# Kernel tuning notes

Hardware: AMD Instinct MI355X
Metric: run time of the kernel (lower is better)

## Reference

```python
import jax, jax.numpy as jnp
import numpy as np

IMG = 64
STEPS = 10
UNITS = 256
PATCH_DIM = (IMG // 2) * (IMG // 2) * 9  # 3x3 patches, stride 2, SAME
ENC_IN = PATCH_DIM + 2 * UNITS  # read_window (patch+h_dec) concat h_dec again


def lstm_cell(x, h, c, kernel, rec, bias):
    # Keras LSTMCell gate order: i, f, g(candidate), o
    z = x @ kernel + h @ rec + bias
    i, f, g, o = jnp.split(z, 4, axis=-1)
    c_new = jax.nn.sigmoid(f) * c + jax.nn.sigmoid(i) * jnp.tanh(g)
    h_new = jax.nn.sigmoid(o) * jnp.tanh(c_new)
    return h_new, c_new


def extract_patches(img):
    # img: [B, H, W] -> 3x3 patches, stride 2, SAME -> [B, (H/2)*(W/2)*9]
    p = jax.lax.conv_general_dilated_patches(
        img[:, None, :, :], (3, 3), (2, 2), 'SAME')  # [B, 9, H/2, W/2]
    p = jnp.transpose(p, (0, 2, 3, 1))  # TF extract_patches layout [B,H',W',9]
    return p.reshape(img.shape[0], -1)


def setup_inputs() -> dict:
    key = jax.random.key(0)
    ks = jax.random.split(key, 8)
    B = 512
    s = 0.05  # small init scale to avoid gate saturation
    return {
        'x': jax.random.uniform(ks[0], (B, IMG, IMG), dtype=jnp.float32),
        'enc_kernel': jax.random.normal(ks[1], (ENC_IN, 4 * UNITS), dtype=jnp.float32) * s,
        'enc_rec': jax.random.normal(ks[2], (UNITS, 4 * UNITS), dtype=jnp.float32) * s,
        'enc_bias': jnp.zeros((4 * UNITS,), jnp.float32),
        'dec_kernel': jax.random.normal(ks[3], (UNITS, 4 * UNITS), dtype=jnp.float32) * s,
        'dec_rec': jax.random.normal(ks[4], (UNITS, 4 * UNITS), dtype=jnp.float32) * s,
        'dec_bias': jnp.zeros((4 * UNITS,), jnp.float32),
        'W_enc': jax.random.normal(ks[5], (UNITS, 10), dtype=jnp.float32) * s,
        'b_enc': jnp.zeros((10,), jnp.float32),
        'W_dec': jax.random.normal(ks[6], (UNITS, IMG * IMG), dtype=jnp.float32) * s,
        'b_dec': jnp.zeros((IMG * IMG,), jnp.float32),
    }


def reference(x, enc_kernel, enc_rec, enc_bias, dec_kernel, dec_rec, dec_bias,
              W_enc, b_enc, W_dec, b_dec):
    B = x.shape[0]
    canvas0 = jnp.zeros((B, IMG, IMG), x.dtype)
    h_enc0 = c_enc0 = h_dec0 = c_dec0 = jnp.zeros((B, UNITS), x.dtype)

    def step(carry, _):
        canvas, h_enc, c_enc, h_dec, c_dec = carry
        x_hat = x - jax.nn.sigmoid(canvas)                      # error image
        patches = extract_patches(x_hat)                        # [B, PATCH_DIM]
        read_window = jnp.concatenate([patches, h_dec], axis=1)
        enc_in = jnp.concatenate([read_window, h_dec], axis=1)  # [B, ENC_IN]
        h_enc, c_enc = lstm_cell(enc_in, h_enc, c_enc, enc_kernel, enc_rec, enc_bias)
        # attention over 10 slots; glimpse vector as attn-weighted slot embeddings
        attn = jax.nn.softmax(h_enc @ W_enc + b_enc, axis=1)    # [B, 10]
        z = attn @ W_enc.T                                      # [B, UNITS]
        h_dec, c_dec = lstm_cell(z, h_dec, c_dec, dec_kernel, dec_rec, dec_bias)
        canvas = canvas + (h_dec @ W_dec + b_dec).reshape(B, IMG, IMG)
        return (canvas, h_enc, c_enc, h_dec, c_dec), None

    (canvas, _, _, _, _), _ = jax.lax.scan(
        step, (canvas0, h_enc0, c_enc0, h_dec0, c_dec0), None, length=STEPS)
    return canvas
```

## Files before the change

### kernel.cpp

```cpp
#include <hip/hip_runtime.h>

typedef unsigned short ushort_t;
typedef __attribute__((ext_vector_type(8))) short short8;
typedef __attribute__((ext_vector_type(4))) float floatx4;
typedef __attribute__((ext_vector_type(4))) unsigned int uintx4;

#define BSZ   512
#define UNITS 256
#define IMG   64
#define STEPS 10
#define GATES 1024
#define KENC  4608
#define NBLK  256
#define BK 32
#define FLAG_STRIDE 32

__device__ inline float b2f(ushort_t u) {
  union { float f; unsigned int i; } v; v.i = ((unsigned int)u) << 16; return v.f;
}
__device__ inline ushort_t f2b(float f) {
  unsigned int u = __float_as_uint(f);
  u += 0x7fffu + ((u >> 16) & 1u);
  return (ushort_t)(u >> 16);
}
__device__ inline float sigm(float x) { return 1.f / (1.f + __expf(-x)); }

#define GLL(g, l) __builtin_amdgcn_global_load_lds(                      \
    (const __attribute__((address_space(1))) void*)(g),                  \
    (__attribute__((address_space(3))) void*)(l), 16, 0, 0)

#define CLOADF(p)    __hip_atomic_load((p), __ATOMIC_RELAXED, __HIP_MEMORY_SCOPE_AGENT)
#define CSTOREF(p,v) __hip_atomic_store((p), (v), __ATOMIC_RELAXED, __HIP_MEMORY_SCOPE_AGENT)
#define CSTOREU(p,v) __hip_atomic_store((p), (ushort_t)(v), __ATOMIC_RELAXED, __HIP_MEMORY_SCOPE_AGENT)

__device__ inline uintx4 cload16(const ushort_t* p) {
  uintx4 r;
  asm volatile("global_load_dwordx4 %0, %1, off sc0 sc1" : "=v"(r) : "v"(p));
  return r;
}
__device__ inline void waitvm0() {
  asm volatile("s_waitcnt vmcnt(0)" ::: "memory");
}
__device__ inline unsigned ldsaddr(const ushort_t* p) {
  return (unsigned)(unsigned long long)(const __attribute__((address_space(3))) void*)p;
}
__device__ inline void dsw16(unsigned off, uintx4 v) {
  asm volatile("ds_write_b128 %0, %1" :: "v"(off), "v"(v));
}

__device__ inline void gridbar(unsigned* bar, unsigned id) {
  __syncthreads();
  const int b = blockIdx.x, t = threadIdx.x;
  unsigned* gen = bar + NBLK * FLAG_STRIDE;
  if (b == 0) {
    if (t > 0 && t < NBLK) {
      while (__hip_atomic_load(bar + t * FLAG_STRIDE, __ATOMIC_RELAXED,
                               __HIP_MEMORY_SCOPE_AGENT) < id)
        __builtin_amdgcn_s_sleep(1);
    }
    __syncthreads();
    if (t == 0)
      __hip_atomic_store(gen, id, __ATOMIC_RELAXED, __HIP_MEMORY_SCOPE_AGENT);
  } else if (t == 0) {
    __hip_atomic_store(bar + b * FLAG_STRIDE, id, __ATOMIC_RELAXED,
                       __HIP_MEMORY_SCOPE_AGENT);
    while (__hip_atomic_load(gen, __ATOMIC_RELAXED,
                             __HIP_MEMORY_SCOPE_AGENT) < id)
      __builtin_amdgcn_s_sleep(1);
  }
  __syncthreads();
}

__global__ __launch_bounds__(256) void k_prep_pix(const float* __restrict__ ek,
                                                  ushort_t* __restrict__ ohi) {
  __shared__ float T[64][68];
  int t = threadIdx.x;
  int pix0 = blockIdx.x * 64, n0 = blockIdx.y * 64;
  int r = t >> 2, seg = t & 3;
  int pix = pix0 + r;
  int ri = pix >> 6, ci = pix & 63;
  float4 acc4[4];
#pragma unroll
  for (int j = 0; j < 4; ++j) acc4[j] = float4{0.f, 0.f, 0.f, 0.f};
#pragma unroll
  for (int di = 0; di < 3; ++di) {
    int ii = ri - di;
    if (ii < 0 || (ii & 1)) continue;
    int oi = ii >> 1;  if (oi >= 32) continue;
#pragma unroll
    for (int dj = 0; dj < 3; ++dj) {
      int jj = ci - dj;
      if (jj < 0 || (jj & 1)) continue;
      int oj = jj >> 1;  if (oj >= 32) continue;
      const float* row = ek + (size_t)((oi * 32 + oj) * 9 + di * 3 + dj) * GATES
                         + n0 + seg * 16;
#pragma unroll
      for (int j = 0; j < 4; ++j) {
        float4 v = *(const float4*)(row + j * 4);
        acc4[j].x += v.x; acc4[j].y += v.y; acc4[j].z += v.z; acc4[j].w += v.w;
      }
    }
  }
#pragma unroll
  for (int j = 0; j < 4; ++j) *(float4*)&T[r][seg * 16 + j * 4] = acc4[j];
  __syncthreads();
  ushort_t thi[16];
#pragma unroll
  for (int j = 0; j < 16; ++j) thi[j] = f2b(T[seg * 16 + j][r]);
  size_t off = (size_t)(n0 + r) * KENC + pix0 + seg * 16;
  *(uint4*)(ohi + off)     = *(const uint4*)&thi[0];
  *(uint4*)(ohi + off + 8) = *(const uint4*)&thi[8];
}

__global__ __launch_bounds__(256) void k_prep_multi(
    const float* __restrict__ ek, const float* __restrict__ er,
    const float* __restrict__ dk, const float* __restrict__ dr,
    const float* __restrict__ Wdec,
    ushort_t* __restrict__ Wet_hi,
    ushort_t* __restrict__ Wdt_hi, ushort_t* __restrict__ Wdt_lo,
    ushort_t* __restrict__ Wct_hi, ushort_t* __restrict__ Wct_lo,
    unsigned* __restrict__ bar) {
  __shared__ float T[64][68];
  int t = threadIdx.x;
  int z = blockIdx.z;
  int k0 = blockIdx.x * 64, n0 = blockIdx.y * 64;
  int r = t >> 2, seg = t & 3;
  if (z == 0) {
    int fid = (blockIdx.y * 4 + blockIdx.x) * 256 + t;
    if (fid <= NBLK * FLAG_STRIDE) bar[fid] = 0u;
  }

  const float *s0, *s1 = nullptr;
  ushort_t *ohi, *olo = nullptr;
  int src_ld, out_ld, koff;
  if (z == 0) { s0 = ek + (size_t)9216 * GATES; s1 = ek + (size_t)9472 * GATES;
                src_ld = GATES; ohi = Wet_hi; out_ld = KENC; koff = 4096; }
  else if (z == 1) { s0 = er; src_ld = GATES; ohi = Wet_hi; out_ld = KENC; koff = 4352; }
  else if (z == 2) { s0 = dk; src_ld = GATES; ohi = Wdt_hi; olo = Wdt_lo; out_ld = 512; koff = 0; }
  else if (z == 3) { s0 = dr; src_ld = GATES; ohi = Wdt_hi; olo = Wdt_lo; out_ld = 512; koff = 256; }
  else { s0 = Wdec; src_ld = 4096; ohi = Wct_hi; olo = Wct_lo; out_ld = 256; koff = 0;
         n0 += (z - 4) * 1024; }

  const float* src = s0 + (size_t)(k0 + r) * src_ld + n0 + seg * 16;
  const float* src2 = s1 ? (s1 + (size_t)(k0 + r) * src_ld + n0 + seg * 16) : nullptr;
#pragma unroll
  for (int j = 0; j < 4; ++j) {
    float4 v = *(const float4*)(src + j * 4);
    if (src2) {
      float4 w = *(const float4*)(src2 + j * 4);
      v.x += w.x; v.y += w.y; v.z += w.z; v.w += w.w;
    }
    *(float4*)&T[r][seg * 16 + j * 4] = v;
  }
  __syncthreads();
  ushort_t thi[16], tlo[16];
#pragma unroll
  for (int j = 0; j < 16; ++j) {
    float v = T[seg * 16 + j][r];
    ushort_t h = f2b(v);
    thi[j] = h;
    tlo[j] = f2b(v - b2f(h));
  }
  size_t off = (size_t)(n0 + r) * out_ld + koff + k0 + seg * 16;
  *(uint4*)(ohi + off)     = *(const uint4*)&thi[0];
  *(uint4*)(ohi + off + 8) = *(const uint4*)&thi[8];
  if (olo) {
    *(uint4*)(olo + off)     = *(const uint4*)&tlo[0];
    *(uint4*)(olo + off + 8) = *(const uint4*)&tlo[8];
  }
}

__global__ __launch_bounds__(512, 2) void k_persist(
    const float* __restrict__ x,
    const float* __restrict__ ebias, const float* __restrict__ dbias,
    const float* __restrict__ Wenc, const float* __restrict__ benc,
    const float* __restrict__ bdec,
    float* __restrict__ canvas, float* __restrict__ c_enc, float* __restrict__ c_dec,
    float* __restrict__ zep,
    ushort_t* __restrict__ ehi, ushort_t* __restrict__ dhi, ushort_t* __restrict__ dlo,
    const ushort_t* __restrict__ Wet_hi,
    const ushort_t* __restrict__ Wdt_hi, const ushort_t* __restrict__ Wdt_lo,
    const ushort_t* __restrict__ Wct_hi, const ushort_t* __restrict__ Wct_lo,
    unsigned* bar) {
  __shared__ __align__(16) ushort_t smem[24576];
  const int b = blockIdx.x, t = threadIdx.x;
  const int lane = t & 63, w = t >> 6;
  const int q = lane >> 4, c16 = lane & 15;
  const int qs = (q ^ ((c16 >> 1) & 3)) * 8;
  const int half = t >> 8, u8 = t & 255;
  const int rrow = b * 2 + half;
  unsigned barid = 0;

  {
    const int cby = b >> 5, cbx = b & 31;
    float4* cv4 = (float4*)canvas;
    const float4 z4 = float4{0.f, 0.f, 0.f, 0.f};
#pragma unroll
    for (int j = 0; j < 4; ++j) {
      int idx = j * 512 + t;
      cv4[(size_t)(cby * 64 + (idx >> 5)) * 1024 + cbx * 32 + (idx & 31)] = z4;
    }
    c_enc[rrow * UNITS + u8] = 0.f;
    if (b < 128) {
      const int m0 = (b >> 3) * 32, u0 = (b & 7) * 32;
#pragma unroll
      for (int j = 0; j < 2; ++j) {
        int idx = j * 512 + t;
        c_dec[(m0 + (idx >> 5)) * UNITS + u0 + (idx & 31)] = 0.f;
      }
    }
    CSTOREU(ehi + (size_t)rrow * KENC + 4096 + u8, 0);
    CSTOREU(ehi + (size_t)rrow * KENC + 4352 + u8, 0);
    CSTOREU(dhi + (size_t)rrow * 512 + u8, 0);
    CSTOREU(dhi + (size_t)rrow * 512 + 256 + u8, 0);
    CSTOREU(dlo + (size_t)rrow * 512 + u8, 0);
    CSTOREU(dlo + (size_t)rrow * 512 + 256 + u8, 0);
    for (int pix = u8; pix < 4096; pix += 256)
      CSTOREU(ehi + (size_t)rrow * KENC + pix,
              f2b(x[(size_t)rrow * 4096 + pix] - 0.5f));
  }
  gridbar(bar, ++barid);

  for (int s = 0; s < STEPS; ++s) {
    {
      const int bm = b & 15, bu = (b >> 4) & 3, bz = b >> 6;
      const int m0 = bm * 32, u0 = bu * 64, kstart = bz * 1152;
      const int sseg = (t & 3) ^ ((t >> 3) & 3);
      const ushort_t* pA = ehi + (size_t)(m0 + ((t >> 2) & 31)) * KENC
                           + kstart + sseg * 8;
      const int br0 = t >> 2, br1 = 128 + (t >> 2);
      const int g0 = (br0 >> 6) * 256 + u0 + (br0 & 63);
      const int g1 = (br1 >> 6) * 256 + u0 + (br1 & 63);
      const ushort_t* pB0 = Wet_hi + (size_t)g0 * KENC + kstart + sseg * 8;
      const ushort_t* pB1 = Wet_hi + (size_t)g1 * KENC + kstart + sseg * 8;

      floatx4 acc[2][2];
#pragma unroll
      for (int i = 0; i < 2; ++i)
#pragma unroll
        for (int j = 0; j < 2; ++j) acc[i][j] = floatx4{0.f, 0.f, 0.f, 0.f};

      uintx4 va;
      if (t < 128) va = cload16(pA);
      GLL(pB0, &smem[1024 + t * 8]);
      GLL(pB1, &smem[5120 + t * 8]);
      pA += BK; pB0 += BK; pB1 += BK;
      waitvm0();
      if (t < 128) dsw16(ldsaddr(&smem[t * 8]), va);
      __syncthreads();
      for (int kt = 0; kt < 36; ++kt) {
        const int cur = (kt & 1) * 9216, nxt = 9216 - cur;
        if (kt + 1 < 36) {
          if (t < 128) va = cload16(pA);
          GLL(pB0, &smem[nxt + 1024 + t * 8]);
          GLL(pB1, &smem[nxt + 5120 + t * 8]);
          pA += BK; pB0 += BK; pB1 += BK;
        }
        short8 af[2], bf[2];
#pragma unroll
        for (int i = 0; i < 2; ++i)
          af[i] = *(const short8*)&smem[cur + (i * 16 + c16) * BK + qs];
#pragma unroll
        for (int j = 0; j < 2; ++j)
          bf[j] = *(const short8*)&smem[cur + 1024 + (w * 32 + j * 16 + c16) * BK + qs];
#pragma unroll
        for (int mi = 0; mi < 2; ++mi)
#pragma unroll
          for (int ni = 0; ni < 2; ++ni)
            acc[mi][ni] = __builtin_amdgcn_mfma_f32_16x16x32_bf16(af[mi], bf[ni], acc[mi][ni], 0, 0, 0);
        if (kt + 1 < 36) {
          waitvm0();
          if (t < 128) dsw16(ldsaddr(&smem[nxt + t * 8]), va);
        }
        __syncthreads();
      }
#pragma unroll
      for (int mi = 0; mi < 2; ++mi)
#pragma unroll
        for (int ni = 0; ni < 2; ++ni) {
          const int col = w * 32 + ni * 16 + c16;
          const int gcol = (col >> 6) * 256 + u0 + (col & 63);
          const int rowb = m0 + mi * 16 + q * 4;
#pragma unroll
          for (int r = 0; r < 4; ++r)
            CSTOREF(zep + ((size_t)(rowb + r) * 4 + bz) * 1024 + gcol, acc[mi][ni][r]);
        }
    }
    gridbar(bar, ++barid);

    {
      float* shf = (float*)smem;
      const float* rb = zep + (size_t)rrow * 4096 + u8;
      float v[16];
#pragma unroll
      for (int z = 0; z < 4; ++z)
#pragma unroll
        for (int g = 0; g < 4; ++g)
          v[z * 4 + g] = CLOADF(rb + z * 1024 + g * 256);
      float zi = ebias[u8], zf = ebias[u8 + 256];
      float zg = ebias[u8 + 512], zo = ebias[u8 + 768];
#pragma unroll
      for (int z = 0; z < 4; ++z) {
        zi += v[z * 4]; zf += v[z * 4 + 1]; zg += v[z * 4 + 2]; zo += v[z * 4 + 3];
      }
      float c = c_enc[rrow * UNITS + u8];
      float cn = sigm(zf) * c + sigm(zi) * tanhf(zg);
      float h = sigm(zo) * tanhf(cn);
      c_enc[rrow * UNITS + u8] = cn;
      CSTOREU(ehi + (size_t)rrow * KENC + 4352 + u8, f2b(h));
      shf[half * 256 + u8] = h;
      __syncthreads();
      if (u8 < 64) {
        float acc[10];
#pragma unroll
        for (int j = 0; j < 10; ++j) acc[j] = 0.f;
        for (int qq = 0; qq < 4; ++qq) {
          float hv = shf[half * 256 + u8 + qq * 64];
          const float* wr = Wenc + (u8 + qq * 64) * 10;
#pragma unroll
          for (int j = 0; j < 10; ++j) acc[j] += hv * wr[j];
        }
        for (int off = 32; off > 0; off >>= 1)
#pragma unroll
          for (int j = 0; j < 10; ++j) acc[j] += __shfl_down(acc[j], off);
        if (u8 == 0)
          for (int j = 0; j < 10; ++j) shf[512 + half * 10 + j] = acc[j] + benc[j];
      }
      __syncthreads();
      float mx = shf[512 + half * 10];
      for (int j = 1; j < 10; ++j) mx = fmaxf(mx, shf[512 + half * 10 + j]);
      float e[10], se = 0.f;
      for (int j = 0; j < 10; ++j) { e[j] = __expf(shf[512 + half * 10 + j] - mx); se += e[j]; }
      float inv = 1.f / se;
      const float* wr = Wenc + u8 * 10;
      float zzv = 0.f;
      for (int j = 0; j < 10; ++j) zzv += e[j] * inv * wr[j];
      ushort_t zh = f2b(zzv);
      CSTOREU(dhi + (size_t)rrow * 512 + u8, zh);
      CSTOREU(dlo + (size_t)rrow * 512 + u8, f2b(zzv - b2f(zh)));
    }
    gridbar(bar, ++barid);

    if (b < 128) {
      const int m0 = (b >> 3) * 32, u0 = (b & 7) * 32;
      const int wm = w >> 2, wn = w & 3;
      const int ta2 = t & 127;
      const int sseg = (ta2 & 3) ^ ((ta2 >> 3) & 3);
      const ushort_t* pA = ((t < 128) ? dhi : dlo)
                           + (size_t)(m0 + (ta2 >> 2)) * 512 + sseg * 8;
      const int brow = t >> 2;
      const int gD = (brow >> 5) * 256 + u0 + (brow & 31);
      const int bsegD = (t & 3) ^ ((t >> 3) & 3);
      const ushort_t* pBh = Wdt_hi + (size_t)gD * 512 + bsegD * 8;
      const ushort_t* pBl = Wdt_lo + (size_t)gD * 512 + bsegD * 8;
      const int dA = ((t < 128) ? 0 : 1024) + ta2 * 8;

      floatx4 acc[2];
      acc[0] = floatx4{0.f, 0.f, 0.f, 0.f};
      acc[1] = floatx4{0.f, 0.f, 0.f, 0.f};

      uintx4 va;
      if (t < 256) va = cload16(pA);
      GLL(pBh, &smem[2048 + t * 8]);
      GLL(pBl, &smem[6144 + t * 8]);
      pA += BK; pBh += BK; pBl += BK;
      waitvm0();
      if (t < 256) dsw16(ldsaddr(&smem[dA]), va);
      __syncthreads();
      for (int kt = 0; kt < 16; ++kt) {
        const int cur = (kt & 1) * 10240, nxt = 10240 - cur;
        if (kt + 1 < 16) {
          if (t < 256) va = cload16(pA);
          GLL(pBh, &smem[nxt + 2048 + t * 8]);
          GLL(pBl, &smem[nxt + 6144 + t * 8]);
          pA += BK; pBh += BK; pBl += BK;
        }
        short8 ah, al, bh[2], bl[2];
        {
          const int ra = (wm * 16 + c16) * BK + qs;
          ah = *(const short8*)&smem[cur + ra];
          al = *(const short8*)&smem[cur + 1024 + ra];
        }
#pragma unroll
        for (int i = 0; i < 2; ++i) {
          const int rb2 = (wn * 32 + i * 16 + c16) * BK + qs;
          bh[i] = *(const short8*)&smem[cur + 2048 + rb2];
          bl[i] = *(const short8*)&smem[cur + 6144 + rb2];
        }
#pragma unroll
        for (int ni = 0; ni < 2; ++ni) {
          acc[ni] = __builtin_amdgcn_mfma_f32_16x16x32_bf16(ah, bh[ni], acc[ni], 0, 0, 0);
          acc[ni] = __builtin_amdgcn_mfma_f32_16x16x32_bf16(ah, bl[ni], acc[ni], 0, 0, 0);
          acc[ni] = __builtin_amdgcn_mfma_f32_16x16x32_bf16(al, bh[ni], acc[ni], 0, 0, 0);
        }
        if (kt + 1 < 16) {
          waitvm0();
          if (t < 256) dsw16(ldsaddr(&smem[nxt + dA]), va);
        }
        __syncthreads();
      }
      float* zacc = (float*)smem;
#pragma unroll
      for (int ni = 0; ni < 2; ++ni) {
        const int col = wn * 32 + ni * 16 + c16;
        const int rowb = wm * 16 + q * 4;
#pragma unroll
        for (int r = 0; r < 4; ++r) zacc[(rowb + r) * 128 + col] = acc[ni][r];
      }
      __syncthreads();
#pragma unroll
      for (int j = 0; j < 2; ++j) {
        const int idx = j * 512 + t;
        const int row = idx >> 5, uu = idx & 31;
        const int un = u0 + uu, rg = m0 + row;
        float zi = zacc[row * 128 + uu]      + dbias[un];
        float zf = zacc[row * 128 + 32 + uu] + dbias[256 + un];
        float zg = zacc[row * 128 + 64 + uu] + dbias[512 + un];
        float zo = zacc[row * 128 + 96 + uu] + dbias[768 + un];
        float c = c_dec[rg * UNITS + un];
        float cn = sigm(zf) * c + sigm(zi) * tanhf(zg);
        float h = sigm(zo) * tanhf(cn);
        c_dec[rg * UNITS + un] = cn;
        ushort_t hh = f2b(h);
        CSTOREU(dhi + (size_t)rg * 512 + 256 + un, hh);
        CSTOREU(dlo + (size_t)rg * 512 + 256 + un, f2b(h - b2f(hh)));
        CSTOREU(ehi + (size_t)rg * KENC + 4096 + un, hh);
      }
    }
    gridbar(bar, ++barid);

    {
      const int by = b >> 5, bx = b & 31;
      const int m0 = by * 64, n0 = bx * 128;
      const int wm = w >> 2, wn = w & 3;
      const int ia = t & 255;
      const int aseg = ((ia & 3) ^ ((ia >> 3) & 3));
      const int bseg = ((t & 3) ^ ((t >> 3) & 3));
      const ushort_t* pA = ((t < 256) ? (dhi + 256) : (dlo + 256))
                           + (size_t)(m0 + (ia >> 2)) * 512 + aseg * 8;
      const ushort_t* pBh = Wct_hi + (size_t)(n0 + (t >> 2)) * 256 + bseg * 8;
      const ushort_t* pBl = Wct_lo + (size_t)(n0 + (t >> 2)) * 256 + bseg * 8;
      const int dA = ((t < 256) ? 0 : 2048) + ia * 8;

      floatx4 acc[2][2];
#pragma unroll
      for (int i = 0; i < 2; ++i)
#pragma unroll
        for (int j = 0; j < 2; ++j) acc[i][j] = floatx4{0.f, 0.f, 0.f, 0.f};

      uintx4 va = cload16(pA);
      GLL(pBh, &smem[4096 + t * 8]);
      GLL(pBl, &smem[8192 + t * 8]);
      pA += BK; pBh += BK; pBl += BK;
      waitvm0();
      dsw16(ldsaddr(&smem[dA]), va);
      __syncthreads();
      for (int kt = 0; kt < 8; ++kt) {
        const int cur = (kt & 1) * 12288, nxt = 12288 - cur;
        if (kt + 1 < 8) {
          va = cload16(pA);
          GLL(pBh, &smem[nxt + 4096 + t * 8]);
          GLL(pBl, &smem[nxt + 8192 + t * 8]);
          pA += BK; pBh += BK; pBl += BK;
        }
        short8 ah[2], al[2], bh[2], bl[2];
#pragma unroll
        for (int i = 0; i < 2; ++i) {
          const int ra = (wm * 32 + i * 16 + c16) * BK + qs;
          ah[i] = *(const short8*)&smem[cur + ra];
          al[i] = *(const short8*)&smem[cur + 2048 + ra];
          const int rb2 = (wn * 32 + i * 16 + c16) * BK + qs;
          bh[i] = *(const short8*)&smem[cur + 4096 + rb2];
          bl[i] = *(const short8*)&smem[cur + 8192 + rb2];
        }
#pragma unroll
        for (int mi = 0; mi < 2; ++mi)
#pragma unroll
          for (int ni = 0; ni < 2; ++ni) {
            acc[mi][ni] = __builtin_amdgcn_mfma_f32_16x16x32_bf16(ah[mi], bh[ni], acc[mi][ni], 0, 0, 0);
            acc[mi][ni] = __builtin_amdgcn_mfma_f32_16x16x32_bf16(ah[mi], bl[ni], acc[mi][ni], 0, 0, 0);
            acc[mi][ni] = __builtin_amdgcn_mfma_f32_16x16x32_bf16(al[mi], bh[ni], acc[mi][ni], 0, 0, 0);
          }
        if (kt + 1 < 8) {
          waitvm0();
          dsw16(ldsaddr(&smem[nxt + dA]), va);
        }
        __syncthreads();
      }
#pragma unroll
      for (int mi = 0; mi < 2; ++mi)
#pragma unroll
        for (int ni = 0; ni < 2; ++ni) {
          const int n = n0 + wn * 32 + ni * 16 + c16;
          const int mb = m0 + wm * 32 + mi * 16 + q * 4;
          const float bv = bdec[n];
#pragma unroll
          for (int r = 0; r < 4; ++r) {
            const int m = mb + r;
            const size_t idx = (size_t)m * 4096 + n;
            const float cv = canvas[idx] + acc[mi][ni][r] + bv;
            canvas[idx] = cv;
            CSTOREU(ehi + (size_t)m * KENC + n, f2b(x[idx] - sigm(cv)));
          }
        }
    }
    if (s + 1 < STEPS) gridbar(bar, ++barid);
  }
}

extern "C" void kernel_launch(void* const* d_in, const int* in_sizes, int n_in,
                              void* d_out, int out_size, void* d_ws, size_t ws_size,
                              hipStream_t stream) {
  const float* x     = (const float*)d_in[0];
  const float* ek    = (const float*)d_in[1];
  const float* er    = (const float*)d_in[2];
  const float* ebias = (const float*)d_in[3];
  const float* dk    = (const float*)d_in[4];
  const float* dr    = (const float*)d_in[5];
  const float* dbias = (const float*)d_in[6];
  const float* Wenc  = (const float*)d_in[7];
  const float* benc  = (const float*)d_in[8];
  const float* Wdec  = (const float*)d_in[9];
  const float* bdec  = (const float*)d_in[10];

  float* canvas = (float*)d_out;

  char* p = (char*)d_ws;
  float* c_enc  = (float*)p;        p += (size_t)BSZ * UNITS * 4;
  float* c_dec  = (float*)p;        p += (size_t)BSZ * UNITS * 4;
  float* zep    = (float*)p;        p += (size_t)4 * BSZ * GATES * 4;
  ushort_t* ehi = (ushort_t*)p;     p += (size_t)BSZ * KENC * 2;
  ushort_t* dhi = (ushort_t*)p;     p += (size_t)BSZ * 512 * 2;
  ushort_t* dlo = (ushort_t*)p;     p += (size_t)BSZ * 512 * 2;
  ushort_t* Wet_hi = (ushort_t*)p;  p += (size_t)GATES * KENC * 2;
  ushort_t* Wdt_hi = (ushort_t*)p;  p += (size_t)GATES * 512 * 2;
  ushort_t* Wdt_lo = (ushort_t*)p;  p += (size_t)GATES * 512 * 2;
  ushort_t* Wct_hi = (ushort_t*)p;  p += (size_t)4096 * UNITS * 2;
  ushort_t* Wct_lo = (ushort_t*)p;  p += (size_t)4096 * UNITS * 2;
  unsigned* bar = (unsigned*)p;     p += (size_t)(NBLK * FLAG_STRIDE + 16) * 4;

  k_prep_pix<<<dim3(64, 16), 256, 0, stream>>>(ek, Wet_hi);
  k_prep_multi<<<dim3(4, 16, 8), 256, 0, stream>>>(ek, er, dk, dr, Wdec,
                                                   Wet_hi, Wdt_hi, Wdt_lo,
                                                   Wct_hi, Wct_lo, bar);

  void* args[] = {(void*)&x, (void*)&ebias, (void*)&dbias, (void*)&Wenc,
                  (void*)&benc, (void*)&bdec, (void*)&canvas, (void*)&c_enc,
                  (void*)&c_dec, (void*)&zep, (void*)&ehi,
                  (void*)&dhi, (void*)&dlo, (void*)&Wet_hi, (void*)&Wdt_hi,
                  (void*)&Wdt_lo, (void*)&Wct_hi, (void*)&Wct_lo, (void*)&bar};
  if (hipLaunchCooperativeKernel((void*)k_persist, dim3(NBLK), dim3(512),
                                 args, 0, stream) != hipSuccess) {
    k_persist<<<dim3(NBLK), dim3(512), 0, stream>>>(
        x, ebias, dbias, Wenc, benc, bdec, canvas, c_enc, c_dec, zep,
        ehi, dhi, dlo, Wet_hi, Wdt_hi, Wdt_lo, Wct_hi, Wct_lo, bar);
  }
}
```

Baseline: 838.6 us.

## Retile persistent kernel GEMM phases for all blocks and vectorized gate reads

```diff
diff --git a/kernel.cpp b/kernel.cpp
--- a/kernel.cpp
+++ b/kernel.cpp
@@ -182,7 +182,7 @@
     const ushort_t* __restrict__ Wdt_hi, const ushort_t* __restrict__ Wdt_lo,
     const ushort_t* __restrict__ Wct_hi, const ushort_t* __restrict__ Wct_lo,
     unsigned* bar) {
-  __shared__ __align__(16) ushort_t smem[24576];
+  __shared__ __align__(16) ushort_t smem[36864];
   const int b = blockIdx.x, t = threadIdx.x;
   const int lane = t & 63, w = t >> 6;
   const int q = lane >> 4, c16 = lane & 15;
@@ -192,23 +192,16 @@
   unsigned barid = 0;
 
   {
-    const int cby = b >> 5, cbx = b & 31;
+    const int cm0 = (b >> 4) * 32, cn0 = (b & 15) * 64;
     float4* cv4 = (float4*)canvas;
     const float4 z4 = float4{0.f, 0.f, 0.f, 0.f};
 #pragma unroll
     for (int j = 0; j < 4; ++j) {
       int idx = j * 512 + t;
-      cv4[(size_t)(cby * 64 + (idx >> 5)) * 1024 + cbx * 32 + (idx & 31)] = z4;
+      cv4[(size_t)(cm0 + (idx >> 6)) * 1024 + cn0 + (idx & 63)] = z4;
     }
     c_enc[rrow * UNITS + u8] = 0.f;
-    if (b < 128) {
-      const int m0 = (b >> 3) * 32, u0 = (b & 7) * 32;
-#pragma unroll
-      for (int j = 0; j < 2; ++j) {
-        int idx = j * 512 + t;
-        c_dec[(m0 + (idx >> 5)) * UNITS + u0 + (idx & 31)] = 0.f;
-      }
-    }
+    c_dec[((b & 31) * 16 + (t >> 5)) * UNITS + (b >> 5) * 32 + (t & 31)] = 0.f;
     CSTOREU(ehi + (size_t)rrow * KENC + 4096 + u8, 0);
     CSTOREU(ehi + (size_t)rrow * KENC + 4352 + u8, 0);
     CSTOREU(dhi + (size_t)rrow * 512 + u8, 0);
@@ -223,86 +216,86 @@
 
   for (int s = 0; s < STEPS; ++s) {
     {
-      const int bm = b & 15, bu = (b >> 4) & 3, bz = b >> 6;
-      const int m0 = bm * 32, u0 = bu * 64, kstart = bz * 1152;
+      const int bm = b & 31, bu = (b >> 5) & 1, bz = b >> 6;
+      const int m0 = bm * 16, kstart = bz * 1152;
       const int sseg = (t & 3) ^ ((t >> 3) & 3);
-      const ushort_t* pA = ehi + (size_t)(m0 + ((t >> 2) & 31)) * KENC
-                           + kstart + sseg * 8;
-      const int br0 = t >> 2, br1 = 128 + (t >> 2);
-      const int g0 = (br0 >> 6) * 256 + u0 + (br0 & 63);
-      const int g1 = (br1 >> 6) * 256 + u0 + (br1 & 63);
-      const ushort_t* pB0 = Wet_hi + (size_t)g0 * KENC + kstart + sseg * 8;
-      const ushort_t* pB1 = Wet_hi + (size_t)g1 * KENC + kstart + sseg * 8;
-
-      floatx4 acc[2][2];
-#pragma unroll
-      for (int i = 0; i < 2; ++i)
-#pragma unroll
-        for (int j = 0; j < 2; ++j) acc[i][j] = floatx4{0.f, 0.f, 0.f, 0.f};
+      const ushort_t* pA = ehi + (size_t)(m0 + (t >> 2)) * KENC + kstart + sseg * 8;
+      const int br = t >> 2;
+      const ushort_t* pB[4];
+#pragma unroll
+      for (int c = 0; c < 4; ++c) {
+        const int r0 = c * 128 + br;
+        const int srow = (r0 >> 7) * 256 + bu * 128 + (r0 & 127);
+        pB[c] = Wet_hi + (size_t)srow * KENC + kstart + sseg * 8;
+      }
+
+      floatx4 acc[4];
+#pragma unroll
+      for (int j = 0; j < 4; ++j) acc[j] = floatx4{0.f, 0.f, 0.f, 0.f};
 
       uintx4 va;
-      if (t < 128) va = cload16(pA);
-      GLL(pB0, &smem[1024 + t * 8]);
-      GLL(pB1, &smem[5120 + t * 8]);
-      pA += BK; pB0 += BK; pB1 += BK;
+      if (t < 64) va = cload16(pA);
+#pragma unroll
+      for (int c = 0; c < 4; ++c) GLL(pB[c], &smem[512 + c * 4096 + t * 8]);
+      pA += BK;
+#pragma unroll
+      for (int c = 0; c < 4; ++c) pB[c] += BK;
       waitvm0();
-      if (t < 128) dsw16(ldsaddr(&smem[t * 8]), va);
+      if (t < 64) dsw16(ldsaddr(&smem[t * 8]), va);
       __syncthreads();
       for (int kt = 0; kt < 36; ++kt) {
-        const int cur = (kt & 1) * 9216, nxt = 9216 - cur;
+        const int cur = (kt & 1) * 16896, nxt = 16896 - cur;
         if (kt + 1 < 36) {
-          if (t < 128) va = cload16(pA);
-          GLL(pB0, &smem[nxt + 1024 + t * 8]);
-          GLL(pB1, &smem[nxt + 5120 + t * 8]);
-          pA += BK; pB0 += BK; pB1 += BK;
-        }
-        short8 af[2], bf[2];
-#pragma unroll
-        for (int i = 0; i < 2; ++i)
-          af[i] = *(const short8*)&smem[cur + (i * 16 + c16) * BK + qs];
-#pragma unroll
-        for (int j = 0; j < 2; ++j)
-          bf[j] = *(const short8*)&smem[cur + 1024 + (w * 32 + j * 16 + c16) * BK + qs];
-#pragma unroll
-        for (int mi = 0; mi < 2; ++mi)
-#pragma unroll
-          for (int ni = 0; ni < 2; ++ni)
-            acc[mi][ni] = __builtin_amdgcn_mfma_f32_16x16x32_bf16(af[mi], bf[ni], acc[mi][ni], 0, 0, 0);
+          if (t < 64) va = cload16(pA);
+#pragma unroll
+          for (int c = 0; c < 4; ++c) GLL(pB[c], &smem[nxt + 512 + c * 4096 + t * 8]);
+          pA += BK;
+#pragma unroll
+          for (int c = 0; c < 4; ++c) pB[c] += BK;
+        }
+        short8 af = *(const short8*)&smem[cur + c16 * BK + qs];
+        short8 bf[4];
+#pragma unroll
+        for (int j = 0; j < 4; ++j)
+          bf[j] = *(const short8*)&smem[cur + 512 + (w * 64 + j * 16 + c16) * BK + qs];
+#pragma unroll
+        for (int j = 0; j < 4; ++j)
+          acc[j] = __builtin_amdgcn_mfma_f32_16x16x32_bf16(af, bf[j], acc[j], 0, 0, 0);
         if (kt + 1 < 36) {
           waitvm0();
-          if (t < 128) dsw16(ldsaddr(&smem[nxt + t * 8]), va);
+          if (t < 64) dsw16(ldsaddr(&smem[nxt + t * 8]), va);
         }
         __syncthreads();
       }
 #pragma unroll
-      for (int mi = 0; mi < 2; ++mi)
-#pragma unroll
-        for (int ni = 0; ni < 2; ++ni) {
-          const int col = w * 32 + ni * 16 + c16;
-          const int gcol = (col >> 6) * 256 + u0 + (col & 63);
-          const int rowb = m0 + mi * 16 + q * 4;
-#pragma unroll
-          for (int r = 0; r < 4; ++r)
-            CSTOREF(zep + ((size_t)(rowb + r) * 4 + bz) * 1024 + gcol, acc[mi][ni][r]);
-        }
+      for (int ni = 0; ni < 4; ++ni) {
+        const int col = w * 64 + ni * 16 + c16;
+        const int g = col >> 7, uu = col & 127;
+        const int unit = bu * 128 + uu;
+#pragma unroll
+        for (int r = 0; r < 4; ++r)
+          CSTOREF(zep + (size_t)(m0 + q * 4 + r) * 4096 + unit * 16 + bz * 4 + g,
+                  acc[ni][r]);
+      }
     }
     gridbar(bar, ++barid);
 
     {
       float* shf = (float*)smem;
-      const float* rb = zep + (size_t)rrow * 4096 + u8;
-      float v[16];
-#pragma unroll
-      for (int z = 0; z < 4; ++z)
-#pragma unroll
-        for (int g = 0; g < 4; ++g)
-          v[z * 4 + g] = CLOADF(rb + z * 1024 + g * 256);
-      float zi = ebias[u8], zf = ebias[u8 + 256];
-      float zg = ebias[u8 + 512], zo = ebias[u8 + 768];
-#pragma unroll
-      for (int z = 0; z < 4; ++z) {
-        zi += v[z * 4]; zf += v[z * 4 + 1]; zg += v[z * 4 + 2]; zo += v[z * 4 + 3];
-      }
+      const float* rb = zep + (size_t)rrow * 4096 + u8 * 16;
+      uintx4 v0 = cload16((const ushort_t*)(rb));
+      uintx4 v1 = cload16((const ushort_t*)(rb + 4));
+      uintx4 v2 = cload16((const ushort_t*)(rb + 8));
+      uintx4 v3 = cload16((const ushort_t*)(rb + 12));
+      waitvm0();
+      float zi = ebias[u8]       + __uint_as_float(v0[0]) + __uint_as_float(v1[0])
+                                 + __uint_as_float(v2[0]) + __uint_as_float(v3[0]);
+      float zf = ebias[u8 + 256] + __uint_as_float(v0[1]) + __uint_as_float(v1[1])
+                                 + __uint_as_float(v2[1]) + __uint_as_float(v3[1]);
+      float zg = ebias[u8 + 512] + __uint_as_float(v0[2]) + __uint_as_float(v1[2])
+                                 + __uint_as_float(v2[2]) + __uint_as_float(v3[2]);
+      float zo = ebias[u8 + 768] + __uint_as_float(v0[3]) + __uint_as_float(v1[3])
+                                 + __uint_as_float(v2[3]) + __uint_as_float(v3[3]);
       float c = c_enc[rrow * UNITS + u8];
       float cn = sigm(zf) * c + sigm(zi) * tanhf(zg);
       float h = sigm(zo) * tanhf(cn);
@@ -341,77 +334,58 @@
     }
     gridbar(bar, ++barid);
 
-    if (b < 128) {
-      const int m0 = (b >> 3) * 32, u0 = (b & 7) * 32;
-      const int wm = w >> 2, wn = w & 3;
-      const int ta2 = t & 127;
-      const int sseg = (ta2 & 3) ^ ((ta2 >> 3) & 3);
-      const ushort_t* pA = ((t < 128) ? dhi : dlo)
-                           + (size_t)(m0 + (ta2 >> 2)) * 512 + sseg * 8;
-      const int brow = t >> 2;
-      const int gD = (brow >> 5) * 256 + u0 + (brow & 31);
+    {
+      const int bm = b & 31, bu = b >> 5;
+      const int m0 = bm * 16, u0 = bu * 32;
+      const int ta = t & 63;
+      const int sseg = (ta & 3) ^ ((ta >> 3) & 3);
+      const ushort_t* pA = ((t < 64) ? dhi : dlo)
+                           + (size_t)(m0 + (ta >> 2)) * 512 + sseg * 8;
+      const int br = t >> 2;
+      const int gsrc = (br >> 5) * 256 + u0 + (br & 31);
       const int bsegD = (t & 3) ^ ((t >> 3) & 3);
-      const ushort_t* pBh = Wdt_hi + (size_t)gD * 512 + bsegD * 8;
-      const ushort_t* pBl = Wdt_lo + (size_t)gD * 512 + bsegD * 8;
-      const int dA = ((t < 128) ? 0 : 1024) + ta2 * 8;
-
-      floatx4 acc[2];
-      acc[0] = floatx4{0.f, 0.f, 0.f, 0.f};
-      acc[1] = floatx4{0.f, 0.f, 0.f, 0.f};
+      const ushort_t* pBh = Wdt_hi + (size_t)gsrc * 512 + bsegD * 8;
+      const ushort_t* pBl = Wdt_lo + (size_t)gsrc * 512 + bsegD * 8;
+      const int dA = ((t < 64) ? 0 : 512) + ta * 8;
+
+      floatx4 acc = floatx4{0.f, 0.f, 0.f, 0.f};
 
       uintx4 va;
-      if (t < 256) va = cload16(pA);
-      GLL(pBh, &smem[2048 + t * 8]);
-      GLL(pBl, &smem[6144 + t * 8]);
+      if (t < 128) va = cload16(pA);
+      GLL(pBh, &smem[1024 + t * 8]);
+      GLL(pBl, &smem[5120 + t * 8]);
       pA += BK; pBh += BK; pBl += BK;
       waitvm0();
-      if (t < 256) dsw16(ldsaddr(&smem[dA]), va);
+      if (t < 128) dsw16(ldsaddr(&smem[dA]), va);
       __syncthreads();
       for (int kt = 0; kt < 16; ++kt) {
-        const int cur = (kt & 1) * 10240, nxt = 10240 - cur;
+        const int cur = (kt & 1) * 9216, nxt = 9216 - cur;
         if (kt + 1 < 16) {
-          if (t < 256) va = cload16(pA);
-          GLL(pBh, &smem[nxt + 2048 + t * 8]);
-          GLL(pBl, &smem[nxt + 6144 + t * 8]);
+          if (t < 128) va = cload16(pA);
+          GLL(pBh, &smem[nxt + 1024 + t * 8]);
+          GLL(pBl, &smem[nxt + 5120 + t * 8]);
           pA += BK; pBh += BK; pBl += BK;
         }
-        short8 ah, al, bh[2], bl[2];
-        {
-          const int ra = (wm * 16 + c16) * BK + qs;
-          ah = *(const short8*)&smem[cur + ra];
-          al = *(const short8*)&smem[cur + 1024 + ra];
-        }
-#pragma unroll
-        for (int i = 0; i < 2; ++i) {
-          const int rb2 = (wn * 32 + i * 16 + c16) * BK + qs;
-          bh[i] = *(const short8*)&smem[cur + 2048 + rb2];
-          bl[i] = *(const short8*)&smem[cur + 6144 + rb2];
-        }
-#pragma unroll
-        for (int ni = 0; ni < 2; ++ni) {
-          acc[ni] = __builtin_amdgcn_mfma_f32_16x16x32_bf16(ah, bh[ni], acc[ni], 0, 0, 0);
-          acc[ni] = __builtin_amdgcn_mfma_f32_16x16x32_bf16(ah, bl[ni], acc[ni], 0, 0, 0);
-          acc[ni] = __builtin_amdgcn_mfma_f32_16x16x32_bf16(al, bh[ni], acc[ni], 0, 0, 0);
-        }
+        short8 ah = *(const short8*)&smem[cur + c16 * BK + qs];
+        short8 al = *(const short8*)&smem[cur + 512 + c16 * BK + qs];
+        short8 bh = *(const short8*)&smem[cur + 1024 + (w * 16 + c16) * BK + qs];
+        short8 bl = *(const short8*)&smem[cur + 5120 + (w * 16 + c16) * BK + qs];
+        acc = __builtin_amdgcn_mfma_f32_16x16x32_bf16(ah, bh, acc, 0, 0, 0);
+        acc = __builtin_amdgcn_mfma_f32_16x16x32_bf16(ah, bl, acc, 0, 0, 0);
+        acc = __builtin_amdgcn_mfma_f32_16x16x32_bf16(al, bh, acc, 0, 0, 0);
         if (kt + 1 < 16) {
           waitvm0();
-          if (t < 256) dsw16(ldsaddr(&smem[nxt + dA]), va);
+          if (t < 128) dsw16(ldsaddr(&smem[nxt + dA]), va);
         }
         __syncthreads();
       }
       float* zacc = (float*)smem;
 #pragma unroll
-      for (int ni = 0; ni < 2; ++ni) {
-        const int col = wn * 32 + ni * 16 + c16;
-        const int rowb = wm * 16 + q * 4;
-#pragma unroll
-        for (int r = 0; r < 4; ++r) zacc[(rowb + r) * 128 + col] = acc[ni][r];
-      }
+      for (int r = 0; r < 4; ++r)
+        zacc[(q * 4 + r) * 128 + w * 16 + c16] = acc[r];
       __syncthreads();
-#pragma unroll
-      for (int j = 0; j < 2; ++j) {
-        const int idx = j * 512 + t;
-        const int row = idx >> 5, uu = idx & 31;
+      {
+        const int row = t >> 5, uu = t & 31;
         const int un = u0 + uu, rg = m0 + row;
         float zi = zacc[row * 128 + uu]      + dbias[un];
         float zf = zacc[row * 128 + 32 + uu] + dbias[256 + un];
@@ -430,79 +404,79 @@
     gridbar(bar, ++barid);
 
     {
-      const int by = b >> 5, bx = b & 31;
-      const int m0 = by * 64, n0 = bx * 128;
+      const int m0 = (b >> 4) * 32, n0 = (b & 15) * 256;
       const int wm = w >> 2, wn = w & 3;
-      const int ia = t & 255;
-      const int aseg = ((ia & 3) ^ ((ia >> 3) & 3));
-      const int bseg = ((t & 3) ^ ((t >> 3) & 3));
-      const ushort_t* pA = ((t < 256) ? (dhi + 256) : (dlo + 256))
-                           + (size_t)(m0 + (ia >> 2)) * 512 + aseg * 8;
-      const ushort_t* pBh = Wct_hi + (size_t)(n0 + (t >> 2)) * 256 + bseg * 8;
-      const ushort_t* pBl = Wct_lo + (size_t)(n0 + (t >> 2)) * 256 + bseg * 8;
-      const int dA = ((t < 256) ? 0 : 2048) + ia * 8;
-
-      floatx4 acc[2][2];
-#pragma unroll
-      for (int i = 0; i < 2; ++i)
-#pragma unroll
-        for (int j = 0; j < 2; ++j) acc[i][j] = floatx4{0.f, 0.f, 0.f, 0.f};
-
-      uintx4 va = cload16(pA);
-      GLL(pBh, &smem[4096 + t * 8]);
-      GLL(pBl, &smem[8192 + t * 8]);
-      pA += BK; pBh += BK; pBl += BK;
+      const int ta = t & 127;
+      const int aseg = (ta & 3) ^ ((ta >> 3) & 3);
+      const int bseg = (t & 3) ^ ((t >> 3) & 3);
+      const ushort_t* pA = ((t < 128) ? dhi : dlo) + 256
+                           + (size_t)(m0 + (ta >> 2)) * 512 + aseg * 8;
+      const int br = t >> 2;
+      const ushort_t* pBh0 = Wct_hi + (size_t)(n0 + br) * 256 + bseg * 8;
+      const ushort_t* pBh1 = Wct_hi + (size_t)(n0 + 128 + br) * 256 + bseg * 8;
+      const ushort_t* pBl0 = Wct_lo + (size_t)(n0 + br) * 256 + bseg * 8;
+      const ushort_t* pBl1 = Wct_lo + (size_t)(n0 + 128 + br) * 256 + bseg * 8;
+      const int dA = ((t < 128) ? 0 : 1024) + ta * 8;
+
+      floatx4 acc[4];
+#pragma unroll
+      for (int j = 0; j < 4; ++j) acc[j] = floatx4{0.f, 0.f, 0.f, 0.f};
+
+      uintx4 va;
+      if (t < 256) va = cload16(pA);
+      GLL(pBh0, &smem[2048 + t * 8]);
+      GLL(pBh1, &smem[6144 + t * 8]);
+      GLL(pBl0, &smem[10240 + t * 8]);
+      GLL(pBl1, &smem[14336 + t * 8]);
+      pA += BK; pBh0 += BK; pBh1 += BK; pBl0 += BK; pBl1 += BK;
       waitvm0();
-      dsw16(ldsaddr(&smem[dA]), va);
+      if (t < 256) dsw16(ldsaddr(&smem[dA]), va);
       __syncthreads();
       for (int kt = 0; kt < 8; ++kt) {
-        const int cur = (kt & 1) * 12288, nxt = 12288 - cur;
+        const int cur = (kt & 1) * 18432, nxt = 18432 - cur;
         if (kt + 1 < 8) {
-          va = cload16(pA);
-          GLL(pBh, &smem[nxt + 4096 + t * 8]);
-          GLL(pBl, &smem[nxt + 8192 + t * 8]);
-          pA += BK; pBh += BK; pBl += BK;
-        }
-        short8 ah[2], al[2], bh[2], bl[2];
-#pragma unroll
-        for (int i = 0; i < 2; ++i) {
-          const int ra = (wm * 32 + i * 16 + c16) * BK + qs;
-          ah[i] = *(const short8*)&smem[cur + ra];
-          al[i] = *(const short8*)&smem[cur + 2048 + ra];
-          const int rb2 = (wn * 32 + i * 16 + c16) * BK + qs;
-          bh[i] = *(const short8*)&smem[cur + 4096 + rb2];
-          bl[i] = *(const short8*)&smem[cur + 8192 + rb2];
-        }
-#pragma unroll
-        for (int mi = 0; mi < 2; ++mi)
-#pragma unroll
-          for (int ni = 0; ni < 2; ++ni) {
-            acc[mi][ni] = __builtin_amdgcn_mfma_f32_16x16x32_bf16(ah[mi], bh[ni], acc[mi][ni], 0, 0, 0);
-            acc[mi][ni] = __builtin_amdgcn_mfma_f32_16x16x32_bf16(ah[mi], bl[ni], acc[mi][ni], 0, 0, 0);
-            acc[mi][ni] = __builtin_amdgcn_mfma_f32_16x16x32_bf16(al[mi], bh[ni], acc[mi][ni], 0, 0, 0);
-          }
+          if (t < 256) va = cload16(pA);
+          GLL(pBh0, &smem[nxt + 2048 + t * 8]);
+          GLL(pBh1, &smem[nxt + 6144 + t * 8]);
+          GLL(pBl0, &smem[nxt + 10240 + t * 8]);
+          GLL(pBl1, &smem[nxt + 14336 + t * 8]);
+          pA += BK; pBh0 += BK; pBh1 += BK; pBl0 += BK; pBl1 += BK;
+        }
+        short8 ah = *(const short8*)&smem[cur + (wm * 16 + c16) * BK + qs];
+        short8 al = *(const short8*)&smem[cur + 1024 + (wm * 16 + c16) * BK + qs];
+        short8 bh[4], bl[4];
+#pragma unroll
+        for (int j = 0; j < 4; ++j) {
+          const int rb2 = (wn * 64 + j * 16 + c16) * BK + qs;
+          bh[j] = *(const short8*)&smem[cur + 2048 + rb2];
+          bl[j] = *(const short8*)&smem[cur + 10240 + rb2];
+        }
+#pragma unroll
+        for (int j = 0; j < 4; ++j) {
+          acc[j] = __builtin_amdgcn_mfma_f32_16x16x32_bf16(ah, bh[j], acc[j], 0, 0, 0);
+          acc[j] = __builtin_amdgcn_mfma_f32_16x16x32_bf16(ah, bl[j], acc[j], 0, 0, 0);
+          acc[j] = __builtin_amdgcn_mfma_f32_16x16x32_bf16(al, bh[j], acc[j], 0, 0, 0);
+        }
         if (kt + 1 < 8) {
           waitvm0();
-          dsw16(ldsaddr(&smem[nxt + dA]), va);
+          if (t < 256) dsw16(ldsaddr(&smem[nxt + dA]), va);
         }
         __syncthreads();
       }
 #pragma unroll
-      for (int mi = 0; mi < 2; ++mi)
-#pragma unroll
-        for (int ni = 0; ni < 2; ++ni) {
-          const int n = n0 + wn * 32 + ni * 16 + c16;
-          const int mb = m0 + wm * 32 + mi * 16 + q * 4;
-          const float bv = bdec[n];
-#pragma unroll
-          for (int r = 0; r < 4; ++r) {
-            const int m = mb + r;
-            const size_t idx = (size_t)m * 4096 + n;
-            const float cv = canvas[idx] + acc[mi][ni][r] + bv;
-            canvas[idx] = cv;
-            CSTOREU(ehi + (size_t)m * KENC + n, f2b(x[idx] - sigm(cv)));
-          }
-        }
+      for (int j = 0; j < 4; ++j) {
+        const int n = n0 + wn * 64 + j * 16 + c16;
+        const int mb = m0 + wm * 16 + q * 4;
+        const float bv = bdec[n];
+#pragma unroll
+        for (int r = 0; r < 4; ++r) {
+          const int m = mb + r;
+          const size_t idx = (size_t)m * 4096 + n;
+          const float cv = canvas[idx] + acc[j][r] + bv;
+          canvas[idx] = cv;
+          CSTOREU(ehi + (size_t)m * KENC + n, f2b(x[idx] - sigm(cv)));
+        }
+      }
     }
     if (s + 1 < STEPS) gridbar(bar, ++barid);
   }
```

Measured after the change: 1.152 ms. +37.4%, slower.
